# Optimization experiments

Measured on AMD Instinct MI355X. Metric: run time of the kernel, lower is better.

Reference implementation:

```python
import jax, jax.numpy as jnp
import numpy as np

DIM = 256
N = 262144
LN_EPS = 1e-5


def setup_inputs() -> dict:
    key = jax.random.key(0)
    ks = jax.random.split(key, 16)
    d = DIM
    inp = {
        "x": jax.random.normal(ks[0], (N, d), dtype=jnp.float32),
        # main cell params (torch Linear stores weight as [out, in])
        "W_slow": jax.random.normal(ks[1], (d, d), dtype=jnp.float32) / np.sqrt(d),
        "V_slow": jax.random.normal(ks[2], (d, d), dtype=jnp.float32) * (0.1 / np.sqrt(d)),
        "gate_w": jax.random.normal(ks[3], (1, d), dtype=jnp.float32) / np.sqrt(d),
        "gate_b": jnp.zeros((1,), dtype=jnp.float32),
        # homeostatic core: Linear(4,16) -> LN(16) -> Tanh -> Linear(16,8) -> ReLU -> Linear(8,4) -> Sigmoid
        "sens1_w": jax.random.normal(ks[4], (16, 4), dtype=jnp.float32) * 0.5,
        "sens1_b": jnp.zeros((16,), dtype=jnp.float32),
        "ln_g": jnp.ones((16,), dtype=jnp.float32),
        "ln_b": jnp.zeros((16,), dtype=jnp.float32),
        "sens2_w": jax.random.normal(ks[5], (8, 16), dtype=jnp.float32) * 0.25,
        "sens2_b": jnp.zeros((8,), dtype=jnp.float32),
        "act_w": jax.random.normal(ks[6], (4, 8), dtype=jnp.float32) * 0.35,
        "act_b": jnp.zeros((4,), dtype=jnp.float32),
        # persistent Hebbian memory buffer
        "semantic_memory": jax.random.normal(ks[7], (d, d), dtype=jnp.float32) * 0.01,
    }
    return inp


def _homeostatic_controls(x, h_raw, w_norm, sens1_w, sens1_b, ln_g, ln_b,
                          sens2_w, sens2_b, act_w, act_b):
    # state vector: [surprise, excitation, fatigue, coherence]  -> [N, 4]
    surprise = jnp.abs(jnp.var(x, axis=1) - 0.5)          # unbiased=False variance
    excitation = jnp.mean(jnp.abs(h_raw), axis=1)
    fatigue = jnp.full_like(surprise, w_norm)
    coherence = jnp.full_like(surprise, 0.5)              # loss_val is None
    state = jnp.stack([surprise, excitation, fatigue, coherence], axis=1)
    z = state @ sens1_w.T + sens1_b                        # [N,16]
    mu = jnp.mean(z, axis=-1, keepdims=True)
    var = jnp.mean((z - mu) ** 2, axis=-1, keepdims=True)
    z = (z - mu) * jax.lax.rsqrt(var + LN_EPS) * ln_g + ln_b
    z = jnp.tanh(z)
    z = jax.nn.relu(z @ sens2_w.T + sens2_b)               # [N,8]
    controls = jax.nn.sigmoid(z @ act_w.T + act_b)         # [N,4]
    return controls


def reference(x, W_slow, V_slow, gate_w, gate_b,
              sens1_w, sens1_b, ln_g, ln_b, sens2_w, sens2_b, act_w, act_b,
              semantic_memory):
    # v = clamp(V_slow(x), -2, 2)
    v = jnp.clip(x @ V_slow.T, -2.0, 2.0)                  # [N, d]

    # homeostatic core (no_grad in torch)
    h_raw = x @ W_slow.T
    w_norm = jnp.linalg.norm(W_slow)
    controls = _homeostatic_controls(x, h_raw, w_norm, sens1_w, sens1_b,
                                     ln_g, ln_b, sens2_w, sens2_b, act_w, act_b)
    metabolic_rate = jnp.mean(controls[:, 0])
    gate_value = jnp.mean(controls[:, 2])

    gate = jax.nn.sigmoid(v @ gate_w.T + gate_b) * gate_value  # [N,1]
    output = jnp.clip(gate * v, -2.0, 2.0)

    # training-mode Hebbian memory update (no_grad in torch)
    batch = x.shape[0]
    hebb = (v.T @ x) / batch                               # [d, d]
    forget = jnp.mean(v ** 2, axis=0)[:, None] * semantic_memory
    delta = jnp.tanh(hebb - forget)
    mem = semantic_memory + delta * metabolic_rate * 0.1
    mem_norm = jnp.maximum(jnp.linalg.norm(mem), 1e-6)
    new_memory = mem / mem_norm * 0.5

    return output, new_memory
```

## Files before the change

### kernel.cpp

```cpp
#include <hip/hip_runtime.h>
#include <hip/hip_bf16.h>


#define NTOK 262144

typedef short s16x4 __attribute__((ext_vector_type(4)));
typedef short s16x8 __attribute__((ext_vector_type(8)));
typedef float f32x4 __attribute__((ext_vector_type(4)));
typedef unsigned int u32x4 __attribute__((ext_vector_type(4)));
typedef __bf16 bf16x8 __attribute__((ext_vector_type(8)));

static __device__ __forceinline__ float b2f(short s) {
  unsigned int u = ((unsigned int)(unsigned short)s) << 16;
  return __builtin_bit_cast(float, u);
}
static __device__ __forceinline__ short f2b(float f) {
  __hip_bfloat16 h = __float2bfloat16(f);
  return (short)__builtin_bit_cast(unsigned short, h);
}
static __device__ __forceinline__ float clip2(float f) {
  return fminf(2.f, fmaxf(-2.f, f));
}
static __device__ __forceinline__ unsigned int packu(short lo, short hi) {
  return (unsigned int)(unsigned short)lo | ((unsigned int)(unsigned short)hi << 16);
}
static __device__ __forceinline__ f32x4 mfma16(s16x8 a, s16x8 b, f32x4 c) {
  return __builtin_amdgcn_mfma_f32_16x16x32_bf16(
      __builtin_bit_cast(bf16x8, a), __builtin_bit_cast(bf16x8, b), c, 0, 0, 0);
}

__global__ __launch_bounds__(1024) void k_prep(const float* __restrict__ V,
                                               const float* __restrict__ W,
                                               short* __restrict__ Vb,
                                               short* __restrict__ Wb,
                                               float* __restrict__ scal) {
  int t = blockIdx.x * 1024 + threadIdx.x;
  f32x4 v4 = *(const f32x4*)(V + (size_t)t * 4);
  f32x4 w4 = *(const f32x4*)(W + (size_t)t * 4);
  s16x4 vb, wb;
  float s = 0.f;
#pragma unroll
  for (int e = 0; e < 4; ++e) {
    vb[e] = f2b(v4[e]);
    wb[e] = f2b(w4[e]);
    s += w4[e] * w4[e];
  }
  *(s16x4*)(Vb + (size_t)t * 4) = vb;
  *(s16x4*)(Wb + (size_t)t * 4) = wb;
#pragma unroll
  for (int d = 1; d < 64; d <<= 1) s += __shfl_xor(s, d);
  __shared__ float r[16];
  if ((threadIdx.x & 63) == 0) r[threadIdx.x >> 6] = s;
  __syncthreads();
  if (threadIdx.x == 0) {
    float tt = 0.f;
#pragma unroll
    for (int i = 0; i < 16; ++i) tt += r[i];
    atomicAdd(&scal[0], tt);
  }
}

__global__ __launch_bounds__(256, 2) void k_main(
    const float* __restrict__ x, const short* __restrict__ Vb,
    const short* __restrict__ Wb, const float* __restrict__ gw,
    const float* __restrict__ gb, const float* __restrict__ s1w,
    const float* __restrict__ s1b, const float* __restrict__ lng,
    const float* __restrict__ lnb, const float* __restrict__ s2w,
    const float* __restrict__ s2b, const float* __restrict__ aw,
    const float* __restrict__ ab, short* __restrict__ v_out,
    float* __restrict__ g_out, float* __restrict__ scal) {
  __shared__ __align__(16) short xs[64 * 40];
  __shared__ float red[256];
  int tid = threadIdx.x;
  int lane = tid & 63, wc = tid >> 6;
  int lr = lane & 15, lg = lane >> 4;
  size_t r0 = (size_t)blockIdx.x * 64;

  f32x4 accv[4][4] = {};
  f32x4 acch[4][4] = {};
  float sx = 0.f, sxx = 0.f;
  int srow = tid >> 2, skc = tid & 3;

  const short* vbase = Vb + (size_t)(wc * 64 + lr) * 256 + lg * 8;
  const short* wbase = Wb + (size_t)(wc * 64 + lr) * 256 + lg * 8;
  const float* xsrc = x + (r0 + srow) * 256 + skc * 8;

  f32x4 rxa, rxb;
  rxa = *(const f32x4*)(xsrc);
  rxb = *(const f32x4*)(xsrc + 4);

  for (int ks = 0; ks < 8; ++ks) {
    {
      s16x8 c;
#pragma unroll
      for (int e = 0; e < 4; ++e) {
        float f0 = rxa[e], f1 = rxb[e];
        sx += f0 + f1;
        sxx += f0 * f0 + f1 * f1;
        c[e] = f2b(f0);
        c[4 + e] = f2b(f1);
      }
      *(s16x8*)(xs + srow * 40 + skc * 8) = c;
    }
    __syncthreads();
    if (ks < 7) {
      const float* src = xsrc + (ks + 1) * 32;
      rxa = *(const f32x4*)(src);
      rxb = *(const f32x4*)(src + 4);
    }
    int k0 = ks * 32;
    s16x8 bv[4], bw[4];
#pragma unroll
    for (int nf = 0; nf < 4; ++nf) {
      bv[nf] = *(const s16x8*)(vbase + nf * 16 * 256 + k0);
      bw[nf] = *(const s16x8*)(wbase + nf * 16 * 256 + k0);
    }
#pragma unroll
    for (int mf = 0; mf < 4; ++mf) {
      s16x8 a = *(const s16x8*)(xs + (mf * 16 + lr) * 40 + lg * 8);
#pragma unroll
      for (int nf = 0; nf < 4; ++nf) {
        accv[mf][nf] = mfma16(a, bv[nf], accv[mf][nf]);
        acch[mf][nf] = mfma16(a, bw[nf], acch[mf][nf]);
      }
    }
    __syncthreads();
  }

  float gw4[4];
#pragma unroll
  for (int nf = 0; nf < 4; ++nf) gw4[nf] = gw[wc * 64 + nf * 16 + lr];
  float gd[4][4], hb[4][4];
#pragma unroll
  for (int mf = 0; mf < 4; ++mf)
#pragma unroll
    for (int e = 0; e < 4; ++e) { gd[mf][e] = 0.f; hb[mf][e] = 0.f; }
#pragma unroll
  for (int mf = 0; mf < 4; ++mf)
#pragma unroll
    for (int nf = 0; nf < 4; ++nf)
#pragma unroll
      for (int e = 0; e < 4; ++e) {
        float v = clip2(accv[mf][nf][e]);
        accv[mf][nf][e] = v;
        gd[mf][e] += v * gw4[nf];
        hb[mf][e] += fabsf(acch[mf][nf][e]);
      }
#pragma unroll
  for (int d = 1; d < 16; d <<= 1)
#pragma unroll
    for (int mf = 0; mf < 4; ++mf)
#pragma unroll
      for (int e = 0; e < 4; ++e) {
        gd[mf][e] += __shfl_xor(gd[mf][e], d);
        hb[mf][e] += __shfl_xor(hb[mf][e], d);
      }
  sx += __shfl_xor(sx, 1); sx += __shfl_xor(sx, 2);
  sxx += __shfl_xor(sxx, 1); sxx += __shfl_xor(sxx, 2);

  if (tid < 128) { red[tid] = 0.f; }
  __syncthreads();
  if (lr == 0) {
#pragma unroll
    for (int mf = 0; mf < 4; ++mf)
#pragma unroll
      for (int e = 0; e < 4; ++e) {
        int row = mf * 16 + lg * 4 + e;
        atomicAdd(&red[row], gd[mf][e]);
        atomicAdd(&red[64 + row], hb[mf][e]);
      }
  }
  if (skc == 0) { red[128 + srow] = sx; red[192 + srow] = sxx; }
#pragma unroll
  for (int mf = 0; mf < 4; ++mf)
#pragma unroll
    for (int nf = 0; nf < 4; ++nf)
#pragma unroll
      for (int e = 0; e < 4; ++e) {
        int row = mf * 16 + lg * 4 + e;
        int col = wc * 64 + nf * 16 + lr;
        v_out[(r0 + row) * 256 + col] = f2b(accv[mf][nf][e]);
      }
  __syncthreads();

  float c0v = 0.f, c2v = 0.f;
  if (tid < 64) {
    int row = tid;
    float mean = red[128 + row] * (1.f / 256.f);
    float var = red[192 + row] * (1.f / 256.f) - mean * mean;
    float st[4];
    st[0] = fabsf(var - 0.5f);
    st[1] = red[64 + row] * (1.f / 256.f);
    st[2] = sqrtf(scal[0]);
    st[3] = 0.5f;
    float z[16];
#pragma unroll
    for (int o = 0; o < 16; ++o) {
      float a = s1b[o];
#pragma unroll
      for (int i = 0; i < 4; ++i) a += s1w[o * 4 + i] * st[i];
      z[o] = a;
    }
    float mu = 0.f;
#pragma unroll
    for (int o = 0; o < 16; ++o) mu += z[o];
    mu *= (1.f / 16.f);
    float vz = 0.f;
#pragma unroll
    for (int o = 0; o < 16; ++o) { float d2 = z[o] - mu; vz += d2 * d2; }
    vz *= (1.f / 16.f);
    float rs = rsqrtf(vz + 1e-5f);
#pragma unroll
    for (int o = 0; o < 16; ++o)
      z[o] = tanhf((z[o] - mu) * rs * lng[o] + lnb[o]);
    float z2[8];
#pragma unroll
    for (int o = 0; o < 8; ++o) {
      float a = s2b[o];
#pragma unroll
      for (int i = 0; i < 16; ++i) a += s2w[o * 16 + i] * z[i];
      z2[o] = fmaxf(a, 0.f);
    }
    float cc[2];
#pragma unroll
    for (int q = 0; q < 2; ++q) {
      int o = q * 2;
      float a = ab[o];
#pragma unroll
      for (int i = 0; i < 8; ++i) a += aw[o * 8 + i] * z2[i];
      cc[q] = 1.f / (1.f + expf(-a));
    }
    c0v = cc[0]; c2v = cc[1];
    float graw = red[row] + gb[0];
    g_out[r0 + row] = 1.f / (1.f + expf(-graw));
  }
#pragma unroll
  for (int d = 1; d < 64; d <<= 1) {
    c0v += __shfl_xor(c0v, d);
    c2v += __shfl_xor(c2v, d);
  }
  if (tid == 0) {
    atomicAdd(&scal[1], c0v);
    atomicAdd(&scal[2], c2v);
  }
}

__global__ __launch_bounds__(512, 2) void k_hebb(
    const float* __restrict__ x, const short* __restrict__ v_in,
    const float* __restrict__ g_sig, const float* __restrict__ scal,
    float* __restrict__ colv2, float* __restrict__ parts,
    float* __restrict__ out0) {
  __shared__ __align__(16) unsigned int ldsT[2 * 256 * 17];
  unsigned int* vT = ldsT;
  unsigned int* xT = ldsT + 256 * 17;
  int tid = threadIdx.x;
  int lane = tid & 63, wid = tid >> 6;
  int lr = lane & 15, lg = lane >> 4;
  int wr = wid >> 2, wc = wid & 3;
  size_t n0 = (size_t)blockIdx.x * 1024;
  float gv = scal[2] * (1.f / 262144.f);

  f32x4 acc[8][4] = {};
  float cv2[8] = {0.f, 0.f, 0.f, 0.f, 0.f, 0.f, 0.f, 0.f};
  int np = tid >> 5, ic = tid & 31, i0 = ic * 8;

  for (int nt = 0; nt < 32; ++nt) {
    size_t nr = n0 + nt * 32 + np * 2;
    s16x8 va = *(const s16x8*)(v_in + nr * 256 + i0);
    s16x8 vb = *(const s16x8*)(v_in + (nr + 1) * 256 + i0);
    f32x4 xa0 = *(const f32x4*)(x + nr * 256 + i0);
    f32x4 xa1 = *(const f32x4*)(x + nr * 256 + i0 + 4);
    f32x4 xb0 = *(const f32x4*)(x + (nr + 1) * 256 + i0);
    f32x4 xb1 = *(const f32x4*)(x + (nr + 1) * 256 + i0 + 4);
    float sa = g_sig[nr] * gv, sb = g_sig[nr + 1] * gv;
    f32x4 oa0, oa1, ob0, ob1;
#pragma unroll
    for (int j = 0; j < 4; ++j) {
      float fa = b2f(va[j]), fA = b2f(va[4 + j]);
      float fb = b2f(vb[j]), fB = b2f(vb[4 + j]);
      cv2[j] += fa * fa + fb * fb;
      cv2[4 + j] += fA * fA + fB * fB;
      oa0[j] = clip2(fa * sa); oa1[j] = clip2(fA * sa);
      ob0[j] = clip2(fb * sb); ob1[j] = clip2(fB * sb);
      vT[(i0 + j) * 17 + np] = packu(va[j], vb[j]);
      vT[(i0 + 4 + j) * 17 + np] = packu(va[4 + j], vb[4 + j]);
      xT[(i0 + j) * 17 + np] = packu(f2b(xa0[j]), f2b(xb0[j]));
      xT[(i0 + 4 + j) * 17 + np] = packu(f2b(xa1[j]), f2b(xb1[j]));
    }
    *(f32x4*)(out0 + nr * 256 + i0) = oa0;
    *(f32x4*)(out0 + nr * 256 + i0 + 4) = oa1;
    *(f32x4*)(out0 + (nr + 1) * 256 + i0) = ob0;
    *(f32x4*)(out0 + (nr + 1) * 256 + i0 + 4) = ob1;
    __syncthreads();
    int npb = lg * 4;
    s16x8 bfr[4];
#pragma unroll
    for (int nf = 0; nf < 4; ++nf) {
      int j = wc * 64 + nf * 16 + lr;
      u32x4 q;
      q[0] = xT[j * 17 + npb]; q[1] = xT[j * 17 + npb + 1];
      q[2] = xT[j * 17 + npb + 2]; q[3] = xT[j * 17 + npb + 3];
      bfr[nf] = __builtin_bit_cast(s16x8, q);
    }
#pragma unroll
    for (int mf = 0; mf < 8; ++mf) {
      int i = wr * 128 + mf * 16 + lr;
      u32x4 q;
      q[0] = vT[i * 17 + npb]; q[1] = vT[i * 17 + npb + 1];
      q[2] = vT[i * 17 + npb + 2]; q[3] = vT[i * 17 + npb + 3];
      s16x8 afr = __builtin_bit_cast(s16x8, q);
#pragma unroll
      for (int nf = 0; nf < 4; ++nf)
        acc[mf][nf] = mfma16(afr, bfr[nf], acc[mf][nf]);
    }
    __syncthreads();
  }
  float* myp = parts + (size_t)blockIdx.x * 65536;
#pragma unroll
  for (int mf = 0; mf < 8; ++mf)
#pragma unroll
    for (int nf = 0; nf < 4; ++nf)
#pragma unroll
      for (int e = 0; e < 4; ++e) {
        int i = wr * 128 + mf * 16 + lg * 4 + e;
        int j = wc * 64 + nf * 16 + lr;
        myp[i * 256 + j] = acc[mf][nf][e];
      }
  __syncthreads();
  float* cred = (float*)ldsT;
  if (tid < 256) cred[tid] = 0.f;
  __syncthreads();
#pragma unroll
  for (int j = 0; j < 8; ++j) atomicAdd(&cred[i0 + j], cv2[j]);
  __syncthreads();
  if (tid < 256) atomicAdd(&colv2[tid], cred[tid]);
}

__global__ __launch_bounds__(256) void k_mem1(
    const float* __restrict__ parts, const float* __restrict__ colv2,
    const float* __restrict__ sm, float* __restrict__ mem,
    float* __restrict__ scal) {
  int i = blockIdx.x, j = threadIdx.x;
  float hebb = 0.f;
#pragma unroll 8
  for (int p = 0; p < 256; ++p) hebb += parts[(size_t)p * 65536 + i * 256 + j];
  hebb *= (1.f / 262144.f);
  float mr = scal[1] * (1.f / 262144.f);
  float smv = sm[i * 256 + j];
  float forget = colv2[i] * (1.f / 262144.f) * smv;
  float delta = tanhf(hebb - forget);
  float m = smv + delta * mr * 0.1f;
  mem[i * 256 + j] = m;
  float s = m * m;
#pragma unroll
  for (int d = 1; d < 64; d <<= 1) s += __shfl_xor(s, d);
  __shared__ float r4[4];
  if ((j & 63) == 0) r4[j >> 6] = s;
  __syncthreads();
  if (j == 0) atomicAdd(&scal[3], r4[0] + r4[1] + r4[2] + r4[3]);
}

__global__ __launch_bounds__(256) void k_mem2(const float* __restrict__ mem,
                                              const float* __restrict__ scal,
                                              float* __restrict__ out1) {
  int idx = blockIdx.x * 256 + threadIdx.x;
  float scale = 0.5f / fmaxf(sqrtf(scal[3]), 1e-6f);
  out1[idx] = mem[idx] * scale;
}

extern "C" void kernel_launch(void* const* d_in, const int* in_sizes, int n_in,
                              void* d_out, int out_size, void* d_ws, size_t ws_size,
                              hipStream_t stream) {
  (void)in_sizes; (void)n_in; (void)out_size; (void)ws_size;
  const float* x   = (const float*)d_in[0];
  const float* Wm  = (const float*)d_in[1];
  const float* Vm  = (const float*)d_in[2];
  const float* gw  = (const float*)d_in[3];
  const float* gb  = (const float*)d_in[4];
  const float* s1w = (const float*)d_in[5];
  const float* s1b = (const float*)d_in[6];
  const float* lng = (const float*)d_in[7];
  const float* lnb = (const float*)d_in[8];
  const float* s2w = (const float*)d_in[9];
  const float* s2b = (const float*)d_in[10];
  const float* aw  = (const float*)d_in[11];
  const float* ab  = (const float*)d_in[12];
  const float* sm  = (const float*)d_in[13];
  float* out0 = (float*)d_out;
  float* out1 = out0 + (size_t)NTOK * 256;

  char* w = (char*)d_ws;
  short* v_ws  = (short*)w;
  float* g_ws  = (float*)(w + 134217728);
  float* scal  = (float*)(w + 135266304);
  float* colv2 = (float*)(w + 135266560);
  float* mem   = (float*)(w + 135267584);
  float* parts = (float*)(w + 135529728);
  short* Vb    = (short*)(w + 202638592);
  short* Wb    = (short*)(w + 202769664);

  hipMemsetAsync(scal, 0, 1280, stream);
  k_prep<<<16, 1024, 0, stream>>>(Vm, Wm, Vb, Wb, scal);
  k_main<<<4096, 256, 0, stream>>>(x, Vb, Wb, gw, gb, s1w, s1b, lng, lnb,
                                   s2w, s2b, aw, ab, v_ws, g_ws, scal);
  k_hebb<<<256, 512, 0, stream>>>(x, v_ws, g_ws, scal, colv2, parts, out0);
  k_mem1<<<256, 256, 0, stream>>>(parts, colv2, sm, mem, scal);
  k_mem2<<<256, 256, 0, stream>>>(mem, scal, out1);
}
```

Measured before the change: 400.8 us.

## Split V and W GEMMs across separate waves with 512-thread blocks

Result: no change. 408.8 us (+2.0%).

```diff
diff --git a/kernel.cpp b/kernel.cpp
--- a/kernel.cpp
+++ b/kernel.cpp
@@ -60,7 +60,7 @@
   }
 }
 
-__global__ __launch_bounds__(256, 2) void k_main(
+__global__ __launch_bounds__(512) void k_main(
     const float* __restrict__ x, const short* __restrict__ Vb,
     const short* __restrict__ Wb, const float* __restrict__ gw,
     const float* __restrict__ gb, const float* __restrict__ s1w,
@@ -72,93 +72,96 @@
   __shared__ __align__(16) short xs[64 * 40];
   __shared__ float red[256];
   int tid = threadIdx.x;
-  int lane = tid & 63, wc = tid >> 6;
+  int lane = tid & 63, wid = tid >> 6;
   int lr = lane & 15, lg = lane >> 4;
+  int mat = wid >> 2, wc = wid & 3;
   size_t r0 = (size_t)blockIdx.x * 64;
 
-  f32x4 accv[4][4] = {};
-  f32x4 acch[4][4] = {};
+  f32x4 acc[4][4] = {};
   float sx = 0.f, sxx = 0.f;
-  int srow = tid >> 2, skc = tid & 3;
-
-  const short* vbase = Vb + (size_t)(wc * 64 + lr) * 256 + lg * 8;
-  const short* wbase = Wb + (size_t)(wc * 64 + lr) * 256 + lg * 8;
-  const float* xsrc = x + (r0 + srow) * 256 + skc * 8;
-
-  f32x4 rxa, rxb;
-  rxa = *(const f32x4*)(xsrc);
-  rxb = *(const f32x4*)(xsrc + 4);
-
+  int srow = tid >> 3, skc = tid & 7;
+
+  const short* Bm = mat ? Wb : Vb;
+  const short* bbase = Bm + (size_t)(wc * 64 + lr) * 256 + lg * 8;
+  const float* xsrc = x + (r0 + srow) * 256 + skc * 4;
+
+  f32x4 rx = *(const f32x4*)(xsrc);
+  s16x8 bcur[4], bnext[4];
+#pragma unroll
+  for (int nf = 0; nf < 4; ++nf)
+    bcur[nf] = *(const s16x8*)(bbase + nf * 16 * 256);
+
+#pragma unroll
   for (int ks = 0; ks < 8; ++ks) {
     {
-      s16x8 c;
+      s16x4 c;
 #pragma unroll
       for (int e = 0; e < 4; ++e) {
-        float f0 = rxa[e], f1 = rxb[e];
-        sx += f0 + f1;
-        sxx += f0 * f0 + f1 * f1;
-        c[e] = f2b(f0);
-        c[4 + e] = f2b(f1);
+        float f = rx[e];
+        sx += f;
+        sxx += f * f;
+        c[e] = f2b(f);
       }
-      *(s16x8*)(xs + srow * 40 + skc * 8) = c;
+      *(s16x4*)(xs + srow * 40 + skc * 4) = c;
     }
     __syncthreads();
     if (ks < 7) {
-      const float* src = xsrc + (ks + 1) * 32;
-      rxa = *(const f32x4*)(src);
-      rxb = *(const f32x4*)(src + 4);
-    }
-    int k0 = ks * 32;
-    s16x8 bv[4], bw[4];
-#pragma unroll
-    for (int nf = 0; nf < 4; ++nf) {
-      bv[nf] = *(const s16x8*)(vbase + nf * 16 * 256 + k0);
-      bw[nf] = *(const s16x8*)(wbase + nf * 16 * 256 + k0);
+      rx = *(const f32x4*)(xsrc + (ks + 1) * 32);
+#pragma unroll
+      for (int nf = 0; nf < 4; ++nf)
+        bnext[nf] = *(const s16x8*)(bbase + nf * 16 * 256 + (ks + 1) * 32);
     }
 #pragma unroll
     for (int mf = 0; mf < 4; ++mf) {
       s16x8 a = *(const s16x8*)(xs + (mf * 16 + lr) * 40 + lg * 8);
 #pragma unroll
-      for (int nf = 0; nf < 4; ++nf) {
-        accv[mf][nf] = mfma16(a, bv[nf], accv[mf][nf]);
-        acch[mf][nf] = mfma16(a, bw[nf], acch[mf][nf]);
+      for (int nf = 0; nf < 4; ++nf)
+        acc[mf][nf] = mfma16(a, bcur[nf], acc[mf][nf]);
+    }
+    __syncthreads();
+#pragma unroll
+    for (int nf = 0; nf < 4; ++nf) bcur[nf] = bnext[nf];
+  }
+
+  float pl[4][4];
+  if (mat == 0) {
+    float gw4[4];
+#pragma unroll
+    for (int nf = 0; nf < 4; ++nf) gw4[nf] = gw[wc * 64 + nf * 16 + lr];
+#pragma unroll
+    for (int mf = 0; mf < 4; ++mf)
+#pragma unroll
+      for (int e = 0; e < 4; ++e) {
+        float g = 0.f;
+#pragma unroll
+        for (int nf = 0; nf < 4; ++nf) {
+          float v = clip2(acc[mf][nf][e]);
+          acc[mf][nf][e] = v;
+          g += v * gw4[nf];
+        }
+        pl[mf][e] = g;
       }
-    }
-    __syncthreads();
-  }
-
-  float gw4[4];
-#pragma unroll
-  for (int nf = 0; nf < 4; ++nf) gw4[nf] = gw[wc * 64 + nf * 16 + lr];
-  float gd[4][4], hb[4][4];
-#pragma unroll
-  for (int mf = 0; mf < 4; ++mf)
-#pragma unroll
-    for (int e = 0; e < 4; ++e) { gd[mf][e] = 0.f; hb[mf][e] = 0.f; }
-#pragma unroll
-  for (int mf = 0; mf < 4; ++mf)
-#pragma unroll
-    for (int nf = 0; nf < 4; ++nf)
+  } else {
+#pragma unroll
+    for (int mf = 0; mf < 4; ++mf)
 #pragma unroll
       for (int e = 0; e < 4; ++e) {
-        float v = clip2(accv[mf][nf][e]);
-        accv[mf][nf][e] = v;
-        gd[mf][e] += v * gw4[nf];
-        hb[mf][e] += fabsf(acch[mf][nf][e]);
+        float hbs = 0.f;
+#pragma unroll
+        for (int nf = 0; nf < 4; ++nf) hbs += fabsf(acc[mf][nf][e]);
+        pl[mf][e] = hbs;
       }
+  }
 #pragma unroll
   for (int d = 1; d < 16; d <<= 1)
 #pragma unroll
     for (int mf = 0; mf < 4; ++mf)
 #pragma unroll
-      for (int e = 0; e < 4; ++e) {
-        gd[mf][e] += __shfl_xor(gd[mf][e], d);
-        hb[mf][e] += __shfl_xor(hb[mf][e], d);
-      }
-  sx += __shfl_xor(sx, 1); sx += __shfl_xor(sx, 2);
-  sxx += __shfl_xor(sxx, 1); sxx += __shfl_xor(sxx, 2);
-
-  if (tid < 128) { red[tid] = 0.f; }
+      for (int e = 0; e < 4; ++e) pl[mf][e] += __shfl_xor(pl[mf][e], d);
+  sx += __shfl_xor(sx, 1); sx += __shfl_xor(sx, 2); sx += __shfl_xor(sx, 4);
+  sxx += __shfl_xor(sxx, 1); sxx += __shfl_xor(sxx, 2); sxx += __shfl_xor(sxx, 4);
+
+  if (tid < 128) red[tid] = 0.f;
   __syncthreads();
   if (lr == 0) {
 #pragma unroll
@@ -166,21 +169,22 @@
 #pragma unroll
       for (int e = 0; e < 4; ++e) {
         int row = mf * 16 + lg * 4 + e;
-        atomicAdd(&red[row], gd[mf][e]);
-        atomicAdd(&red[64 + row], hb[mf][e]);
+        atomicAdd(&red[mat * 64 + row], pl[mf][e]);
       }
   }
-  if (skc == 0) { red[128 + srow] = sx; red[192 + srow] = sxx; }
-#pragma unroll
-  for (int mf = 0; mf < 4; ++mf)
-#pragma unroll
-    for (int nf = 0; nf < 4; ++nf)
-#pragma unroll
-      for (int e = 0; e < 4; ++e) {
-        int row = mf * 16 + lg * 4 + e;
-        int col = wc * 64 + nf * 16 + lr;
-        v_out[(r0 + row) * 256 + col] = f2b(accv[mf][nf][e]);
-      }
+  if ((tid & 7) == 0) { red[128 + srow] = sx; red[192 + srow] = sxx; }
+  if (mat == 0) {
+#pragma unroll
+    for (int mf = 0; mf < 4; ++mf)
+#pragma unroll
+      for (int nf = 0; nf < 4; ++nf)
+#pragma unroll
+        for (int e = 0; e < 4; ++e) {
+          int row = mf * 16 + lg * 4 + e;
+          int col = wc * 64 + nf * 16 + lr;
+          v_out[(r0 + row) * 256 + col] = f2b(acc[mf][nf][e]);
+        }
+  }
   __syncthreads();
 
   float c0v = 0.f, c2v = 0.f;
@@ -401,7 +405,7 @@
 
   hipMemsetAsync(scal, 0, 1280, stream);
   k_prep<<<16, 1024, 0, stream>>>(Vm, Wm, Vb, Wb, scal);
-  k_main<<<4096, 256, 0, stream>>>(x, Vb, Wb, gw, gb, s1w, s1b, lng, lnb,
+  k_main<<<4096, 512, 0, stream>>>(x, Vb, Wb, gw, gb, s1w, s1b, lng, lnb,
                                    s2w, s2b, aw, ab, v_ws, g_ws, scal);
   k_hebb<<<256, 512, 0, stream>>>(x, v_ws, g_ws, scal, colv2, parts, out0);
   k_mem1<<<256, 256, 0, stream>>>(parts, colv2, sm, mem, scal);
```
